# Kernel optimization log

Hardware: AMD Instinct MI355X
Metric: run time of the kernel (lower is better)

Reference implementation:

```python
import jax, jax.numpy as jnp
import numpy as np

B, T, D, S, ITERS = 32, 4096, 256, 8, 3
SCALE = D ** -0.5
EPS = 1e-8


def _ln(x, g, b):
    mu = jnp.mean(x, axis=-1, keepdims=True)
    var = jnp.var(x, axis=-1, keepdims=True)
    return (x - mu) / jnp.sqrt(var + 1e-5) * g + b


def setup_inputs() -> dict:
    key = jax.random.key(0)
    ks = jax.random.split(key, 16)
    w = lambda k, shp, s=0.02: jax.random.normal(k, shp, jnp.float32) * s
    return {
        "inputs": jax.random.normal(ks[0], (B, T, D), jnp.float32),
        "slots_mu": w(ks[1], (1, 1, D), 0.1),
        "slots_logsigma": w(ks[2], (1, 1, D), 0.1),
        "noise": jax.random.normal(ks[3], (B, S, D), jnp.float32),
        "Wq": w(ks[4], (D, D)),
        "Wk": w(ks[5], (D, D)),
        "Wv": w(ks[6], (D, D)),
        "norm_g": jnp.ones((D,), jnp.float32),
        "norm_b": jnp.zeros((D,), jnp.float32),
        "gru_wih": w(ks[7], (D, 3 * D)),
        "gru_whh": w(ks[8], (D, 3 * D)),
        "gru_bih": jnp.zeros((3 * D,), jnp.float32),
        "gru_bhh": jnp.zeros((3 * D,), jnp.float32),
        "mlp_ng": jnp.ones((D,), jnp.float32),
        "mlp_nb": jnp.zeros((D,), jnp.float32),
        "mlp_w1": w(ks[9], (D, 4 * D)),
        "mlp_b1": jnp.zeros((4 * D,), jnp.float32),
        "mlp_w2": w(ks[10], (4 * D, D)),
        "mlp_b2": jnp.zeros((D,), jnp.float32),
    }


def reference(inputs, slots_mu, slots_logsigma, noise, Wq, Wk, Wv, norm_g, norm_b,
              gru_wih, gru_whh, gru_bih, gru_bhh, mlp_ng, mlp_nb,
              mlp_w1, mlp_b1, mlp_w2, mlp_b2):
    # init slots: mu + sigma * noise, broadcast [1,1,D] -> [B,S,D]
    slots = slots_mu + jnp.exp(slots_logsigma) * noise

    keys = inputs @ Wk      # [B,T,D]
    values = inputs @ Wv    # [B,T,D]

    for _ in range(ITERS):
        slots_prev = slots
        s_n = _ln(slots, norm_g, norm_b)
        q = s_n @ Wq                                    # [B,S,D]
        dots = jnp.einsum('bsd,btd->bst', q, keys) * SCALE
        attn = jax.nn.softmax(dots, axis=1) + EPS       # softmax over slots
        attn = attn / jnp.sum(attn, axis=-1, keepdims=True)
        updates = jnp.einsum('bst,btd->bsd', attn, values)

        # GRUCell: x = updates, h = slots_prev (elementwise over B*S)
        gi = updates @ gru_wih + gru_bih                # [B,S,3D]
        gh = slots_prev @ gru_whh + gru_bhh
        ir, iz, inn = jnp.split(gi, 3, axis=-1)
        hr, hz, hn = jnp.split(gh, 3, axis=-1)
        r = jax.nn.sigmoid(ir + hr)
        z = jax.nn.sigmoid(iz + hz)
        n = jnp.tanh(inn + r * hn)
        slots = (1.0 - z) * n + z * slots_prev

        # pre-norm residual MLP
        h = _ln(slots, mlp_ng, mlp_nb)
        h = jax.nn.relu(h @ mlp_w1 + mlp_b1)
        slots = slots + (h @ mlp_w2 + mlp_b2)

    return slots
```

## Files before the change

### kernel.cpp

```cpp
#include <hip/hip_runtime.h>
#include <stdint.h>

#define B_ 32
#define T_ 4096
#define D_ 256
#define S_ 8
#define ITERS_ 3
#define SCALE_ 0.0625f
#define EPS_ 1e-8f
#define NCH 16
#define CHUNK (T_/NCH)

typedef short short8 __attribute__((ext_vector_type(8)));
typedef float f32x4 __attribute__((ext_vector_type(4)));

__device__ __forceinline__ uint32_t f2bf1(float x){
  union { float f; uint32_t u; } c; c.f = x;
  return (c.u + 0x7fffu + ((c.u >> 16) & 1u)) >> 16;
}
__device__ __forceinline__ uint32_t pack2bf(float a, float b){
  return f2bf1(a) | (f2bf1(b) << 16);
}
__device__ __forceinline__ float bflo(uint32_t u){ union{uint32_t u;float f;} c; c.u = u << 16; return c.f; }
__device__ __forceinline__ float bfhi(uint32_t u){ union{uint32_t u;float f;} c; c.u = u & 0xffff0000u; return c.f; }

__global__ void k_init(const float* __restrict__ mu, const float* __restrict__ ls,
                       const float* __restrict__ noise, float* __restrict__ slots){
  int i = blockIdx.x * 256 + threadIdx.x;
  int d = i & 255;
  slots[i] = mu[d] + __expf(ls[d]) * noise[i];
}

__global__ void k_wconv(const float* __restrict__ Wk, const float* __restrict__ Wv,
                        uint16_t* __restrict__ Wt){
  int n = blockIdx.x;
  int k = threadIdx.x;
  float v = (n < 256) ? Wk[k*256 + n] : Wv[k*256 + (n - 256)];
  Wt[n*256 + k] = (uint16_t)f2bf1(v);
}

__global__ void k_wq(const float* __restrict__ Wq, uint16_t* __restrict__ Wqt){
  int n = blockIdx.x, k = threadIdx.x;
  Wqt[n*256 + k] = (uint16_t)f2bf1(Wq[k*256 + n] * SCALE_);
}

__global__ void k_bcat(const float* __restrict__ wih, const float* __restrict__ whh,
                       uint16_t* __restrict__ Bcat){
  int n = blockIdx.x;
  int k = threadIdx.x;
  float v;
  if (n < 768) v = (k < 256) ? wih[k*768 + n] : whh[(k-256)*768 + n];
  else         v = (k < 256) ? 0.f            : whh[(k-256)*768 + 512 + (n-768)];
  Bcat[(size_t)n*512 + k] = (uint16_t)f2bf1(v);
}

__global__ void k_bc(const float* __restrict__ bih, const float* __restrict__ bhh,
                     float* __restrict__ bc){
  int i = blockIdx.x*256 + threadIdx.x;
  float v;
  if (i < 512) v = bih[i] + bhh[i];
  else if (i < 768) v = bih[i];
  else v = bhh[i - 256];
  bc[i] = v;
}

__global__ void k_w1t(const float* __restrict__ w1, uint16_t* __restrict__ w1t){
  int n = blockIdx.x, k = threadIdx.x;
  w1t[(size_t)n*256 + k] = (uint16_t)f2bf1(w1[(size_t)k*1024 + n]);
}
__global__ void k_w2t(const float* __restrict__ w2, uint16_t* __restrict__ w2t){
  int n = blockIdx.x, k0 = threadIdx.x;
  #pragma unroll
  for (int j = 0; j < 4; ++j){
    int k = j*256 + k0;
    w2t[(size_t)n*1024 + k] = (uint16_t)f2bf1(w2[(size_t)k*256 + n]);
  }
}

#define PPITCH 40
__global__ __launch_bounds__(256) void k_proj(const float* __restrict__ X,
                                              const uint16_t* __restrict__ Wt,
                                              uint16_t* __restrict__ Kp,
                                              uint16_t* __restrict__ Vp){
  __shared__ __align__(16) uint16_t As[128*PPITCH];
  __shared__ __align__(16) uint16_t Bs[128*PPITCH];
  __shared__ __align__(16) uint16_t Cs[128*128];
  int bid = blockIdx.x;
  int x = bid & 7, j = bid >> 3;
  int tau = 512*x + j;
  int mt = tau >> 2;
  int nt = tau & 3;
  int m0 = mt * 128;
  int n0 = nt * 128;
  int tid = threadIdx.x;
  int lane = tid & 63, wid = tid >> 6;
  int wm = wid >> 1, wn = wid & 1;
  int rsel = lane & 15, g = lane >> 4;

  f32x4 acc[4][4];
  for (int a = 0; a < 4; ++a)
    for (int b = 0; b < 4; ++b)
      acc[a][b] = (f32x4){0.f,0.f,0.f,0.f};

  for (int ks = 0; ks < 8; ++ks){
    int k0 = ks*32;
    #pragma unroll
    for (int i = 0; i < 2; ++i){
      int task = i*256 + tid;
      int row = task >> 2, seg = task & 3;
      const float* gp = X + (size_t)(m0 + row)*256 + k0 + seg*8;
      float4 a = *(const float4*)gp;
      float4 b = *(const float4*)(gp + 4);
      uint4 w;
      w.x = pack2bf(a.x, a.y); w.y = pack2bf(a.z, a.w);
      w.z = pack2bf(b.x, b.y); w.w = pack2bf(b.z, b.w);
      *(uint4*)&As[row*PPITCH + seg*8] = w;
    }
    #pragma unroll
    for (int i = 0; i < 2; ++i){
      int task = i*256 + tid;
      int row = task >> 2, seg = task & 3;
      uint4 v = *(const uint4*)(Wt + (size_t)(n0 + row)*256 + k0 + seg*8);
      *(uint4*)&Bs[row*PPITCH + seg*8] = v;
    }
    __syncthreads();
    short8 af[4], bfr[4];
    #pragma unroll
    for (int t = 0; t < 4; ++t)
      af[t] = *(const short8*)&As[(wm*64 + t*16 + rsel)*PPITCH + g*8];
    #pragma unroll
    for (int t = 0; t < 4; ++t)
      bfr[t] = *(const short8*)&Bs[(wn*64 + t*16 + rsel)*PPITCH + g*8];
    #pragma unroll
    for (int a = 0; a < 4; ++a)
      #pragma unroll
      for (int b = 0; b < 4; ++b)
        acc[a][b] = __builtin_amdgcn_mfma_f32_16x16x32_bf16(af[a], bfr[b], acc[a][b], 0, 0, 0);
    __syncthreads();
  }
  #pragma unroll
  for (int a = 0; a < 4; ++a)
    #pragma unroll
    for (int b = 0; b < 4; ++b)
      #pragma unroll
      for (int r = 0; r < 4; ++r){
        int mrow = wm*64 + a*16 + g*4 + r;
        int ncol = wn*64 + b*16 + rsel;
        Cs[mrow*128 + ncol] = (uint16_t)f2bf1(acc[a][b][r]);
      }
  __syncthreads();
  uint16_t* outp = (n0 < 256) ? Kp : Vp;
  int nbase = n0 & 255;
  #pragma unroll
  for (int i = 0; i < 4; ++i){
    int task = i*256 + tid;
    int row = task >> 3, seg = task & 7;
    uint4 v = *(uint4*)&Cs[row*128 + seg*16];
    *(uint4*)&outp[(size_t)(m0 + row)*256 + nbase + seg*16] = v;
  }
}

#define GPIT 40
template<int MODE>
__global__ __launch_bounds__(256) void k_gemm64(const uint16_t* __restrict__ A,
                                                const uint16_t* __restrict__ Bm,
                                                const float* __restrict__ bias,
                                                const float* __restrict__ resid,
                                                float* __restrict__ Cf,
                                                uint16_t* __restrict__ Cb,
                                                int N, int K){
  __shared__ __align__(16) uint16_t As[64*GPIT];
  __shared__ __align__(16) uint16_t Bs[64*GPIT];
  int m0 = blockIdx.y * 64, n0 = blockIdx.x * 64;
  int tid = threadIdx.x, lane = tid & 63, wid = tid >> 6;
  int wm = wid >> 1, wn = wid & 1;
  int rsel = lane & 15, g = lane >> 4;
  f32x4 acc[2][2];
  #pragma unroll
  for (int a = 0; a < 2; ++a)
    #pragma unroll
    for (int b = 0; b < 2; ++b)
      acc[a][b] = (f32x4){0.f,0.f,0.f,0.f};
  int row_s = tid >> 2, seg = tid & 3;
  for (int k0 = 0; k0 < K; k0 += 32){
    *(uint4*)&As[row_s*GPIT + seg*8] = *(const uint4*)(A  + (size_t)(m0+row_s)*K + k0 + seg*8);
    *(uint4*)&Bs[row_s*GPIT + seg*8] = *(const uint4*)(Bm + (size_t)(n0+row_s)*K + k0 + seg*8);
    __syncthreads();
    short8 af[2], bfr[2];
    #pragma unroll
    for (int t = 0; t < 2; ++t)
      af[t]  = *(const short8*)&As[(wm*32 + t*16 + rsel)*GPIT + g*8];
    #pragma unroll
    for (int t = 0; t < 2; ++t)
      bfr[t] = *(const short8*)&Bs[(wn*32 + t*16 + rsel)*GPIT + g*8];
    #pragma unroll
    for (int a = 0; a < 2; ++a)
      #pragma unroll
      for (int b = 0; b < 2; ++b)
        acc[a][b] = __builtin_amdgcn_mfma_f32_16x16x32_bf16(af[a], bfr[b], acc[a][b], 0, 0, 0);
    __syncthreads();
  }
  #pragma unroll
  for (int a = 0; a < 2; ++a)
    #pragma unroll
    for (int b = 0; b < 2; ++b)
      #pragma unroll
      for (int r = 0; r < 4; ++r){
        int mrow = m0 + wm*32 + a*16 + g*4 + r;
        int ncol = n0 + wn*32 + b*16 + rsel;
        float v = acc[a][b][r];
        if (MODE == 0) Cf[(size_t)mrow*N + ncol] = v;
        if (MODE == 1) Cb[(size_t)mrow*N + ncol] = (uint16_t)f2bf1(fmaxf(v + bias[ncol], 0.f));
        if (MODE == 2) Cf[(size_t)mrow*N + ncol] = v + bias[ncol] + resid[(size_t)mrow*N + ncol];
        if (MODE == 3) Cb[(size_t)mrow*N + ncol] = (uint16_t)f2bf1(v);
      }
}

__global__ __launch_bounds__(256) void k_ln(const float* __restrict__ src,
                                            const float* __restrict__ gg,
                                            const float* __restrict__ bb,
                                            uint16_t* __restrict__ dst){
  __shared__ float red[8];
  int row = blockIdx.x, tid = threadIdx.x;
  int lane = tid & 63, wid = tid >> 6;
  float xv = src[row*256 + tid];
  float s1 = xv, s2 = xv*xv;
  #pragma unroll
  for (int d = 32; d; d >>= 1){ s1 += __shfl_down(s1, d, 64); s2 += __shfl_down(s2, d, 64); }
  if (lane == 0){ red[wid] = s1; red[4 + wid] = s2; }
  __syncthreads();
  float mu = (red[0]+red[1]+red[2]+red[3]) * (1.f/256.f);
  float ms = (red[4]+red[5]+red[6]+red[7]) * (1.f/256.f);
  float rstd = rsqrtf(ms - mu*mu + 1e-5f);
  dst[row*256 + tid] = (uint16_t)f2bf1((xv - mu)*rstd*gg[tid] + bb[tid]);
}

__global__ __launch_bounds__(256) void k_gru_pre(const float* __restrict__ upd_part,
                                                 const float* __restrict__ sum_part,
                                                 const float* __restrict__ slots,
                                                 uint16_t* __restrict__ Acat){
  int row = blockIdx.x;
  int b = row >> 3, s = row & 7;
  int d = threadIdx.x;
  float sum = 0.f;
  #pragma unroll
  for (int ch = 0; ch < 16; ++ch) sum += sum_part[(size_t)(b*16 + ch)*8 + s];
  float acc = 0.f;
  #pragma unroll
  for (int ch = 0; ch < 16; ++ch) acc += upd_part[(size_t)(b*16 + ch)*2048 + s*256 + d];
  Acat[(size_t)row*512 + d]       = (uint16_t)f2bf1(acc / sum);
  Acat[(size_t)row*512 + 256 + d] = (uint16_t)f2bf1(slots[row*256 + d]);
}

__global__ __launch_bounds__(256) void k_combine(const float* __restrict__ G,
                                                 const float* __restrict__ bc,
                                                 const float* __restrict__ slots,
                                                 const float* __restrict__ mng,
                                                 const float* __restrict__ mnb,
                                                 float* __restrict__ s2f,
                                                 uint16_t* __restrict__ snb){
  __shared__ float red[8];
  int row = blockIdx.x, c = threadIdx.x;
  int lane = c & 63, wid = c >> 6;
  const float* Gr = G + (size_t)row*1024;
  float r  = 1.f / (1.f + __expf(-(Gr[c]       + bc[c])));
  float z  = 1.f / (1.f + __expf(-(Gr[256 + c] + bc[256 + c])));
  float Gn = Gr[512 + c], Gh = Gr[768 + c];
  float nn = tanhf((Gn - Gh + bc[512 + c]) + r*(Gh + bc[768 + c]));
  float hv = slots[row*256 + c];
  float s2 = (1.f - z)*nn + z*hv;
  s2f[row*256 + c] = s2;
  float p1 = s2, p2 = s2*s2;
  #pragma unroll
  for (int d = 32; d; d >>= 1){ p1 += __shfl_down(p1, d, 64); p2 += __shfl_down(p2, d, 64); }
  if (lane == 0){ red[wid] = p1; red[4 + wid] = p2; }
  __syncthreads();
  float mu = (red[0]+red[1]+red[2]+red[3]) * (1.f/256.f);
  float ms = (red[4]+red[5]+red[6]+red[7]) * (1.f/256.f);
  float rstd = rsqrtf(ms - mu*mu + 1e-5f);
  snb[row*256 + c] = (uint16_t)f2bf1((s2 - mu)*rstd*mng[c] + mnb[c]);
}

__global__ __launch_bounds__(256) void k_attn(const uint16_t* __restrict__ qbf,
                                              const uint16_t* __restrict__ Kp,
                                              const uint16_t* __restrict__ Vp,
                                              float* __restrict__ upd_part,
                                              float* __restrict__ sum_part){
  __shared__ __align__(16) uint16_t qs[16*264];
  __shared__ __align__(16) uint16_t Ks[64*264];
  __shared__ __align__(16) uint32_t attp[64*4];
  __shared__ float red[8*256];
  __shared__ float ssum[8];
  int bid = blockIdx.x;
  int b = bid >> 4, ch = bid & 15;
  int tid = threadIdx.x, lane = tid & 63, wid = tid >> 6;
  {
    const uint32_t* qg = (const uint32_t*)(qbf + (size_t)b*2048);
    uint32_t* qd = (uint32_t*)qs;
    #pragma unroll
    for (int i = 0; i < 4; ++i){
      int idx = i*256 + tid;
      int s = idx >> 7, c = idx & 127;
      qd[s*132 + c] = qg[idx];
    }
    #pragma unroll
    for (int i = 0; i < 5; ++i){
      int idx = i*256 + tid;
      if (idx < 1056) qd[8*132 + idx] = 0u;
    }
  }
  if (tid < 8) ssum[tid] = 0.f;
  __syncthreads();
  short8 aq[8];
  {
    int rs = lane & 15, g = lane >> 4;
    const char* qb = (const char*)qs;
    #pragma unroll
    for (int kk = 0; kk < 8; ++kk)
      aq[kk] = *(const short8*)(qb + rs*528 + kk*64 + g*16);
  }
  float upd[8][4];
  #pragma unroll
  for (int s = 0; s < 8; ++s){ upd[s][0]=0.f; upd[s][1]=0.f; upd[s][2]=0.f; upd[s][3]=0.f; }
  float sp[4] = {0.f,0.f,0.f,0.f};
  int dd = lane * 4;
  int tq = wid;

  for (int st = 0; st < 4; ++st){
    int t0 = ch*CHUNK + st*64;
    {
      const char* kg = (const char*)Kp + ((size_t)(b*T_ + t0) << 9);
      char* kd = (char*)Ks;
      #pragma unroll
      for (int i = 0; i < 8; ++i){
        int task = i*256 + tid;
        int row = task >> 5, seg = task & 31;
        uint4 v = *(const uint4*)(kg + (row << 9) + (seg << 4));
        *(uint4*)(kd + row*528 + seg*16) = v;
      }
    }
    __syncthreads();
    f32x4 dot = (f32x4){0.f,0.f,0.f,0.f};
    int col = lane & 15, g = lane >> 4;
    {
      const char* kb = (const char*)Ks + (wid*16 + col)*528 + g*16;
      #pragma unroll
      for (int kk = 0; kk < 8; ++kk){
        short8 bf = *(const short8*)(kb + kk*64);
        dot = __builtin_amdgcn_mfma_f32_16x16x32_bf16(aq[kk], bf, dot, 0, 0, 0);
      }
    }
    float x0 = dot[0], x1 = dot[1], x2 = dot[2], x3 = dot[3];
    float y0 = __shfl_xor(x0, 16, 64), y1 = __shfl_xor(x1, 16, 64);
    float y2 = __shfl_xor(x2, 16, 64), y3 = __shfl_xor(x3, 16, 64);
    float m = fmaxf(fmaxf(fmaxf(x0,x1), fmaxf(x2,x3)), fmaxf(fmaxf(y0,y1), fmaxf(y2,y3)));
    float e0 = __expf(x0-m), e1 = __expf(x1-m), e2 = __expf(x2-m), e3 = __expf(x3-m);
    float f0 = __expf(y0-m), f1 = __expf(y1-m), f2 = __expf(y2-m), f3 = __expf(y3-m);
    float inv = 1.f / (e0+e1+e2+e3+f0+f1+f2+f3);
    float p0 = e0*inv + EPS_, p1 = e1*inv + EPS_, p2 = e2*inv + EPS_, p3 = e3*inv + EPS_;
    if (g < 2){
      sp[0] += p0; sp[1] += p1; sp[2] += p2; sp[3] += p3;
      int t = wid*16 + col;
      attp[t*4 + g*2 + 0] = pack2bf(p0, p1);
      attp[t*4 + g*2 + 1] = pack2bf(p2, p3);
    }
    __syncthreads();
    {
      const char* vg = (const char*)Vp + ((size_t)(b*T_ + t0) << 9) + (size_t)dd*2;
      #pragma unroll
      for (int tt = 0; tt < 16; ++tt){
        int tl = tq*16 + tt;
        uint2 vv = *(const uint2*)(vg + ((size_t)tl << 9));
        uint4 aa = *(const uint4*)&attp[tl*4];
        float v0 = bflo(vv.x), v1 = bfhi(vv.x), v2 = bflo(vv.y), v3 = bfhi(vv.y);
        float av[8];
        av[0] = bflo(aa.x); av[1] = bfhi(aa.x); av[2] = bflo(aa.y); av[3] = bfhi(aa.y);
        av[4] = bflo(aa.z); av[5] = bfhi(aa.z); av[6] = bflo(aa.w); av[7] = bfhi(aa.w);
        #pragma unroll
        for (int s = 0; s < 8; ++s){
          upd[s][0] = fmaf(av[s], v0, upd[s][0]);
          upd[s][1] = fmaf(av[s], v1, upd[s][1]);
          upd[s][2] = fmaf(av[s], v2, upd[s][2]);
          upd[s][3] = fmaf(av[s], v3, upd[s][3]);
        }
      }
    }
    __syncthreads();
  }
  for (int ph = 0; ph < 4; ++ph){
    if (tq == ph){
      #pragma unroll
      for (int s = 0; s < 8; ++s)
        #pragma unroll
        for (int j2 = 0; j2 < 4; ++j2){
          if (ph == 0) red[s*256 + dd + j2]  = upd[s][j2];
          else         red[s*256 + dd + j2] += upd[s][j2];
        }
    }
    __syncthreads();
  }
  {
    float* up = upd_part + (size_t)bid * 2048;
    #pragma unroll
    for (int i = 0; i < 8; ++i) up[i*256 + tid] = red[i*256 + tid];
  }
  {
    int col = lane & 15, g = lane >> 4;
    #pragma unroll
    for (int dsh = 1; dsh < 16; dsh <<= 1){
      sp[0] += __shfl_xor(sp[0], dsh, 64); sp[1] += __shfl_xor(sp[1], dsh, 64);
      sp[2] += __shfl_xor(sp[2], dsh, 64); sp[3] += __shfl_xor(sp[3], dsh, 64);
    }
    if (col == 0 && g < 2){
      atomicAdd(&ssum[g*4 + 0], sp[0]);
      atomicAdd(&ssum[g*4 + 1], sp[1]);
      atomicAdd(&ssum[g*4 + 2], sp[2]);
      atomicAdd(&ssum[g*4 + 3], sp[3]);
    }
    __syncthreads();
    if (tid < 8) sum_part[(size_t)bid*8 + tid] = ssum[tid];
  }
}

extern "C" void kernel_launch(void* const* d_in, const int* in_sizes, int n_in,
                              void* d_out, int out_size, void* d_ws, size_t ws_size,
                              hipStream_t stream){
  const float* inputs = (const float*)d_in[0];
  const float* mu     = (const float*)d_in[1];
  const float* lsig   = (const float*)d_in[2];
  const float* noise  = (const float*)d_in[3];
  const float* Wq     = (const float*)d_in[4];
  const float* Wk     = (const float*)d_in[5];
  const float* Wv     = (const float*)d_in[6];
  const float* ng     = (const float*)d_in[7];
  const float* nb     = (const float*)d_in[8];
  const float* wih    = (const float*)d_in[9];
  const float* whh    = (const float*)d_in[10];
  const float* bih    = (const float*)d_in[11];
  const float* bhh    = (const float*)d_in[12];
  const float* mng    = (const float*)d_in[13];
  const float* mnb    = (const float*)d_in[14];
  const float* w1     = (const float*)d_in[15];
  const float* b1     = (const float*)d_in[16];
  const float* w2     = (const float*)d_in[17];
  const float* b2     = (const float*)d_in[18];
  float* slots = (float*)d_out;

  char* ws = (char*)d_ws;
  uint16_t* Wt       = (uint16_t*)(ws + 0);
  uint16_t* qbf      = (uint16_t*)(ws + 0x40000);
  float*    sum_part = (float*)   (ws + 0x60000);
  float*    upd_part = (float*)   (ws + 0x64000);
  uint16_t* Wqt      = (uint16_t*)(ws + 0x480000);
  uint16_t* Bcat     = (uint16_t*)(ws + 0x4A0000);
  uint16_t* w1t      = (uint16_t*)(ws + 0x5A0000);
  uint16_t* w2t      = (uint16_t*)(ws + 0x620000);
  float*    bc       = (float*)   (ws + 0x6A0000);
  uint16_t* Acat     = (uint16_t*)(ws + 0x6B0000);
  float*    G        = (float*)   (ws + 0x6F0000);
  uint16_t* snb      = (uint16_t*)(ws + 0x7F0000);
  float*    s2f      = (float*)   (ws + 0x810000);
  uint16_t* h1b      = (uint16_t*)(ws + 0x850000);
  uint16_t* lnb      = (uint16_t*)(ws + 0x8D0000);
  uint16_t* Kp       = (uint16_t*)(ws + 0x1000000);
  uint16_t* Vp       = (uint16_t*)(ws + 0x5000000);

  hipLaunchKernelGGL(k_init,  dim3(256),  dim3(256), 0, stream, mu, lsig, noise, slots);
  hipLaunchKernelGGL(k_wconv, dim3(512),  dim3(256), 0, stream, Wk, Wv, Wt);
  hipLaunchKernelGGL(k_wq,    dim3(256),  dim3(256), 0, stream, Wq, Wqt);
  hipLaunchKernelGGL(k_bcat,  dim3(1024), dim3(512), 0, stream, wih, whh, Bcat);
  hipLaunchKernelGGL(k_bc,    dim3(4),    dim3(256), 0, stream, bih, bhh, bc);
  hipLaunchKernelGGL(k_w1t,   dim3(1024), dim3(256), 0, stream, w1, w1t);
  hipLaunchKernelGGL(k_w2t,   dim3(256),  dim3(256), 0, stream, w2, w2t);
  hipLaunchKernelGGL(k_proj,  dim3(4096), dim3(256), 0, stream, inputs, Wt, Kp, Vp);

  for (int it = 0; it < ITERS_; ++it){
    hipLaunchKernelGGL(k_ln,        dim3(256), dim3(256), 0, stream, slots, ng, nb, lnb);
    hipLaunchKernelGGL(k_gemm64<3>, dim3(4,4),  dim3(256), 0, stream, lnb, Wqt,
                       (const float*)nullptr, (const float*)nullptr, (float*)nullptr, qbf, 256, 256);
    hipLaunchKernelGGL(k_attn,      dim3(512), dim3(256), 0, stream, qbf, Kp, Vp, upd_part, sum_part);
    hipLaunchKernelGGL(k_gru_pre,   dim3(256), dim3(256), 0, stream, upd_part, sum_part, slots, Acat);
    hipLaunchKernelGGL(k_gemm64<0>, dim3(16,4), dim3(256), 0, stream, Acat, Bcat,
                       (const float*)nullptr, (const float*)nullptr, G, (uint16_t*)nullptr, 1024, 512);
    hipLaunchKernelGGL(k_combine,   dim3(256), dim3(256), 0, stream, G, bc, slots, mng, mnb, s2f, snb);
    hipLaunchKernelGGL(k_gemm64<1>, dim3(16,4), dim3(256), 0, stream, snb, w1t,
                       b1, (const float*)nullptr, (float*)nullptr, h1b, 1024, 256);
    hipLaunchKernelGGL(k_gemm64<2>, dim3(4,4),  dim3(256), 0, stream, h1b, w2t,
                       b2, s2f, slots, (uint16_t*)nullptr, 256, 1024);
  }
}
```

Measured before the change: 526.5 us.

## Fuse prep kernels, LN+Q projection, and two-layer MLP; use hardware bf16 convert

Merges the seven weight-preparation and slot-init kernels into one launch. Fuses the layernorm with the Q projection, and the two MLP GEMMs (with ReLU and residual) into single kernels that keep the hidden activations in shared memory. The input conversion in the K/V projection now uses the v_cvt_pk_bf16_f32 instruction instead of software rounding. This cuts kernel launches and global round trips for the small per-iteration stages, but the fused kernels run on only 16 blocks, which limits parallelism.

```diff
diff --git a/kernel.cpp b/kernel.cpp
--- a/kernel.cpp
+++ b/kernel.cpp
@@ -21,59 +21,67 @@
 __device__ __forceinline__ uint32_t pack2bf(float a, float b){
   return f2bf1(a) | (f2bf1(b) << 16);
 }
+__device__ __forceinline__ uint32_t cvtpk2bf(float a, float b){
+  uint32_t r;
+  asm("v_cvt_pk_bf16_f32 %0, %1, %2" : "=v"(r) : "v"(a), "v"(b));
+  return r;
+}
 __device__ __forceinline__ float bflo(uint32_t u){ union{uint32_t u;float f;} c; c.u = u << 16; return c.f; }
 __device__ __forceinline__ float bfhi(uint32_t u){ union{uint32_t u;float f;} c; c.u = u & 0xffff0000u; return c.f; }
 
-__global__ void k_init(const float* __restrict__ mu, const float* __restrict__ ls,
-                       const float* __restrict__ noise, float* __restrict__ slots){
-  int i = blockIdx.x * 256 + threadIdx.x;
-  int d = i & 255;
-  slots[i] = mu[d] + __expf(ls[d]) * noise[i];
-}
-
-__global__ void k_wconv(const float* __restrict__ Wk, const float* __restrict__ Wv,
-                        uint16_t* __restrict__ Wt){
-  int n = blockIdx.x;
-  int k = threadIdx.x;
-  float v = (n < 256) ? Wk[k*256 + n] : Wv[k*256 + (n - 256)];
-  Wt[n*256 + k] = (uint16_t)f2bf1(v);
-}
-
-__global__ void k_wq(const float* __restrict__ Wq, uint16_t* __restrict__ Wqt){
-  int n = blockIdx.x, k = threadIdx.x;
-  Wqt[n*256 + k] = (uint16_t)f2bf1(Wq[k*256 + n] * SCALE_);
-}
-
-__global__ void k_bcat(const float* __restrict__ wih, const float* __restrict__ whh,
-                       uint16_t* __restrict__ Bcat){
-  int n = blockIdx.x;
-  int k = threadIdx.x;
-  float v;
-  if (n < 768) v = (k < 256) ? wih[k*768 + n] : whh[(k-256)*768 + n];
-  else         v = (k < 256) ? 0.f            : whh[(k-256)*768 + 512 + (n-768)];
-  Bcat[(size_t)n*512 + k] = (uint16_t)f2bf1(v);
-}
-
-__global__ void k_bc(const float* __restrict__ bih, const float* __restrict__ bhh,
-                     float* __restrict__ bc){
-  int i = blockIdx.x*256 + threadIdx.x;
-  float v;
-  if (i < 512) v = bih[i] + bhh[i];
-  else if (i < 768) v = bih[i];
-  else v = bhh[i - 256];
-  bc[i] = v;
-}
-
-__global__ void k_w1t(const float* __restrict__ w1, uint16_t* __restrict__ w1t){
-  int n = blockIdx.x, k = threadIdx.x;
-  w1t[(size_t)n*256 + k] = (uint16_t)f2bf1(w1[(size_t)k*1024 + n]);
-}
-__global__ void k_w2t(const float* __restrict__ w2, uint16_t* __restrict__ w2t){
-  int n = blockIdx.x, k0 = threadIdx.x;
-  #pragma unroll
-  for (int j = 0; j < 4; ++j){
-    int k = j*256 + k0;
-    w2t[(size_t)n*1024 + k] = (uint16_t)f2bf1(w2[(size_t)k*256 + n]);
+__global__ __launch_bounds__(256) void k_prep(const float* __restrict__ Wk, const float* __restrict__ Wv,
+                                              const float* __restrict__ Wq,
+                                              const float* __restrict__ wih, const float* __restrict__ whh,
+                                              const float* __restrict__ bih, const float* __restrict__ bhh,
+                                              const float* __restrict__ w1, const float* __restrict__ w2,
+                                              const float* __restrict__ mu, const float* __restrict__ ls,
+                                              const float* __restrict__ noise,
+                                              uint16_t* __restrict__ Wt, uint16_t* __restrict__ Wqt,
+                                              uint16_t* __restrict__ Bcat, float* __restrict__ bc,
+                                              uint16_t* __restrict__ w1t, uint16_t* __restrict__ w2t,
+                                              float* __restrict__ slots){
+  int g = blockIdx.x, tid = threadIdx.x;
+  if (g < 512){
+    int n = g, k = tid;
+    float v = (n < 256) ? Wk[k*256 + n] : Wv[k*256 + (n - 256)];
+    Wt[n*256 + k] = (uint16_t)f2bf1(v);
+  } else if (g < 768){
+    int n = g - 512, k = tid;
+    Wqt[n*256 + k] = (uint16_t)f2bf1(Wq[k*256 + n] * SCALE_);
+  } else if (g < 1792){
+    int n = g - 768;
+    #pragma unroll
+    for (int j = 0; j < 2; ++j){
+      int k = j*256 + tid;
+      float v;
+      if (n < 768) v = (k < 256) ? wih[k*768 + n] : whh[(k-256)*768 + n];
+      else         v = (k < 256) ? 0.f            : whh[(k-256)*768 + 512 + (n-768)];
+      Bcat[(size_t)n*512 + k] = (uint16_t)f2bf1(v);
+    }
+  } else if (g < 1793){
+    #pragma unroll
+    for (int j = 0; j < 4; ++j){
+      int i = j*256 + tid;
+      float v;
+      if (i < 512) v = bih[i] + bhh[i];
+      else if (i < 768) v = bih[i];
+      else v = bhh[i - 256];
+      bc[i] = v;
+    }
+  } else if (g < 2817){
+    int n = g - 1793, k = tid;
+    w1t[(size_t)n*256 + k] = (uint16_t)f2bf1(w1[(size_t)k*1024 + n]);
+  } else if (g < 3073){
+    int n = g - 2817;
+    #pragma unroll
+    for (int j = 0; j < 4; ++j){
+      int k = j*256 + tid;
+      w2t[(size_t)n*1024 + k] = (uint16_t)f2bf1(w2[(size_t)k*256 + n]);
+    }
+  } else {
+    int i = (g - 3073)*256 + tid;
+    int d = i & 255;
+    slots[i] = mu[d] + __expf(ls[d]) * noise[i];
   }
 }
 
@@ -112,8 +120,8 @@
       float4 a = *(const float4*)gp;
       float4 b = *(const float4*)(gp + 4);
       uint4 w;
-      w.x = pack2bf(a.x, a.y); w.y = pack2bf(a.z, a.w);
-      w.z = pack2bf(b.x, b.y); w.w = pack2bf(b.z, b.w);
+      w.x = cvtpk2bf(a.x, a.y); w.y = cvtpk2bf(a.z, a.w);
+      w.z = cvtpk2bf(b.x, b.y); w.w = cvtpk2bf(b.z, b.w);
       *(uint4*)&As[row*PPITCH + seg*8] = w;
     }
     #pragma unroll
@@ -160,17 +168,75 @@
   }
 }
 
+__global__ __launch_bounds__(256) void k_qln(const float* __restrict__ slots,
+                                             const uint16_t* __restrict__ Wqt,
+                                             const float* __restrict__ ng,
+                                             const float* __restrict__ nb,
+                                             uint16_t* __restrict__ qbf){
+  __shared__ __align__(16) uint16_t snl[16*264];
+  int m0 = blockIdx.x * 16;
+  int tid = threadIdx.x;
+  int r = tid >> 4, cs = (tid & 15) * 16;
+  float xv[16];
+  {
+    const float* sp = slots + (size_t)(m0 + r)*256 + cs;
+    #pragma unroll
+    for (int i = 0; i < 4; ++i){
+      float4 v = *(const float4*)(sp + i*4);
+      xv[i*4+0]=v.x; xv[i*4+1]=v.y; xv[i*4+2]=v.z; xv[i*4+3]=v.w;
+    }
+  }
+  float s1 = 0.f, s2 = 0.f;
+  #pragma unroll
+  for (int i = 0; i < 16; ++i){ s1 += xv[i]; s2 += xv[i]*xv[i]; }
+  #pragma unroll
+  for (int m = 1; m < 16; m <<= 1){ s1 += __shfl_xor(s1, m, 64); s2 += __shfl_xor(s2, m, 64); }
+  float mu = s1 * (1.f/256.f);
+  float ms = s2 * (1.f/256.f);
+  float rstd = rsqrtf(ms - mu*mu + 1e-5f);
+  {
+    uint32_t pk[8];
+    #pragma unroll
+    for (int i = 0; i < 8; ++i){
+      float a = (xv[2*i]   - mu)*rstd*ng[cs+2*i]   + nb[cs+2*i];
+      float b = (xv[2*i+1] - mu)*rstd*ng[cs+2*i+1] + nb[cs+2*i+1];
+      pk[i] = pack2bf(a, b);
+    }
+    uint4* dst = (uint4*)&snl[r*264 + cs];
+    dst[0] = (uint4){pk[0],pk[1],pk[2],pk[3]};
+    dst[1] = (uint4){pk[4],pk[5],pk[6],pk[7]};
+  }
+  __syncthreads();
+  int lane = tid & 63, w = tid >> 6;
+  int rsel = lane & 15, g = lane >> 4;
+  short8 aq[8];
+  #pragma unroll
+  for (int kk = 0; kk < 8; ++kk)
+    aq[kk] = *(const short8*)((const char*)snl + rsel*528 + kk*64 + g*16);
+  int n0w = w*64;
+  #pragma unroll
+  for (int nt = 0; nt < 4; ++nt){
+    f32x4 acc = (f32x4){0.f,0.f,0.f,0.f};
+    #pragma unroll
+    for (int kk = 0; kk < 8; ++kk){
+      short8 bfr = *(const short8*)&Wqt[(size_t)(n0w + nt*16 + rsel)*256 + kk*32 + g*8];
+      acc = __builtin_amdgcn_mfma_f32_16x16x32_bf16(aq[kk], bfr, acc, 0, 0, 0);
+    }
+    #pragma unroll
+    for (int r4 = 0; r4 < 4; ++r4){
+      int row = g*4 + r4;
+      qbf[(size_t)(m0 + row)*256 + n0w + nt*16 + rsel] = (uint16_t)f2bf1(acc[r4]);
+    }
+  }
+}
+
 #define GPIT 40
-template<int MODE>
-__global__ __launch_bounds__(256) void k_gemm64(const uint16_t* __restrict__ A,
-                                                const uint16_t* __restrict__ Bm,
-                                                const float* __restrict__ bias,
-                                                const float* __restrict__ resid,
-                                                float* __restrict__ Cf,
-                                                uint16_t* __restrict__ Cb,
-                                                int N, int K){
+__global__ __launch_bounds__(256) void k_gemmG(const uint16_t* __restrict__ A,
+                                               const uint16_t* __restrict__ Bm,
+                                               float* __restrict__ Cf){
   __shared__ __align__(16) uint16_t As[64*GPIT];
   __shared__ __align__(16) uint16_t Bs[64*GPIT];
+  const int N = 1024, K = 512;
   int m0 = blockIdx.y * 64, n0 = blockIdx.x * 64;
   int tid = threadIdx.x, lane = tid & 63, wid = tid >> 6;
   int wm = wid >> 1, wn = wid & 1;
@@ -208,31 +274,8 @@
       for (int r = 0; r < 4; ++r){
         int mrow = m0 + wm*32 + a*16 + g*4 + r;
         int ncol = n0 + wn*32 + b*16 + rsel;
-        float v = acc[a][b][r];
-        if (MODE == 0) Cf[(size_t)mrow*N + ncol] = v;
-        if (MODE == 1) Cb[(size_t)mrow*N + ncol] = (uint16_t)f2bf1(fmaxf(v + bias[ncol], 0.f));
-        if (MODE == 2) Cf[(size_t)mrow*N + ncol] = v + bias[ncol] + resid[(size_t)mrow*N + ncol];
-        if (MODE == 3) Cb[(size_t)mrow*N + ncol] = (uint16_t)f2bf1(v);
+        Cf[(size_t)mrow*N + ncol] = acc[a][b][r];
       }
-}
-
-__global__ __launch_bounds__(256) void k_ln(const float* __restrict__ src,
-                                            const float* __restrict__ gg,
-                                            const float* __restrict__ bb,
-                                            uint16_t* __restrict__ dst){
-  __shared__ float red[8];
-  int row = blockIdx.x, tid = threadIdx.x;
-  int lane = tid & 63, wid = tid >> 6;
-  float xv = src[row*256 + tid];
-  float s1 = xv, s2 = xv*xv;
-  #pragma unroll
-  for (int d = 32; d; d >>= 1){ s1 += __shfl_down(s1, d, 64); s2 += __shfl_down(s2, d, 64); }
-  if (lane == 0){ red[wid] = s1; red[4 + wid] = s2; }
-  __syncthreads();
-  float mu = (red[0]+red[1]+red[2]+red[3]) * (1.f/256.f);
-  float ms = (red[4]+red[5]+red[6]+red[7]) * (1.f/256.f);
-  float rstd = rsqrtf(ms - mu*mu + 1e-5f);
-  dst[row*256 + tid] = (uint16_t)f2bf1((xv - mu)*rstd*gg[tid] + bb[tid]);
 }
 
 __global__ __launch_bounds__(256) void k_gru_pre(const float* __restrict__ upd_part,
@@ -279,6 +322,62 @@
   float ms = (red[4]+red[5]+red[6]+red[7]) * (1.f/256.f);
   float rstd = rsqrtf(ms - mu*mu + 1e-5f);
   snb[row*256 + c] = (uint16_t)f2bf1((s2 - mu)*rstd*mng[c] + mnb[c]);
+}
+
+#define HPIT 1048
+__global__ __launch_bounds__(256) void k_mlp(const uint16_t* __restrict__ snb,
+                                             const uint16_t* __restrict__ w1t,
+                                             const float* __restrict__ b1,
+                                             const uint16_t* __restrict__ w2t,
+                                             const float* __restrict__ b2,
+                                             const float* __restrict__ s2f,
+                                             float* __restrict__ slots){
+  __shared__ __align__(16) uint16_t h1s[16*HPIT];
+  int m0 = blockIdx.x * 16;
+  int tid = threadIdx.x, lane = tid & 63, w = tid >> 6;
+  int rsel = lane & 15, g = lane >> 4;
+  short8 aq[8];
+  #pragma unroll
+  for (int kk = 0; kk < 8; ++kk)
+    aq[kk] = *(const short8*)&snb[(size_t)(m0 + rsel)*256 + kk*32 + g*8];
+  #pragma unroll
+  for (int nt = 0; nt < 16; ++nt){
+    int ncol = w*256 + nt*16 + rsel;
+    f32x4 acc = (f32x4){0.f,0.f,0.f,0.f};
+    #pragma unroll
+    for (int kk = 0; kk < 8; ++kk){
+      short8 bfr = *(const short8*)&w1t[(size_t)ncol*256 + kk*32 + g*8];
+      acc = __builtin_amdgcn_mfma_f32_16x16x32_bf16(aq[kk], bfr, acc, 0, 0, 0);
+    }
+    float bv = b1[ncol];
+    #pragma unroll
+    for (int r4 = 0; r4 < 4; ++r4){
+      int row = g*4 + r4;
+      h1s[row*HPIT + ncol] = (uint16_t)f2bf1(fmaxf(acc[r4] + bv, 0.f));
+    }
+  }
+  __syncthreads();
+  f32x4 acc2[4];
+  #pragma unroll
+  for (int nt = 0; nt < 4; ++nt) acc2[nt] = (f32x4){0.f,0.f,0.f,0.f};
+  for (int kk = 0; kk < 32; ++kk){
+    short8 aq2 = *(const short8*)((const char*)h1s + rsel*2096 + kk*64 + g*16);
+    #pragma unroll
+    for (int nt = 0; nt < 4; ++nt){
+      short8 bfr = *(const short8*)&w2t[(size_t)(w*64 + nt*16 + rsel)*1024 + kk*32 + g*8];
+      acc2[nt] = __builtin_amdgcn_mfma_f32_16x16x32_bf16(aq2, bfr, acc2[nt], 0, 0, 0);
+    }
+  }
+  #pragma unroll
+  for (int nt = 0; nt < 4; ++nt){
+    int ncol = w*64 + nt*16 + rsel;
+    float bv = b2[ncol];
+    #pragma unroll
+    for (int r4 = 0; r4 < 4; ++r4){
+      int row = m0 + g*4 + r4;
+      slots[(size_t)row*256 + ncol] = s2f[(size_t)row*256 + ncol] + acc2[nt][r4] + bv;
+    }
+  }
 }
 
 __global__ __launch_bounds__(256) void k_attn(const uint16_t* __restrict__ qbf,
@@ -460,32 +559,20 @@
   float*    G        = (float*)   (ws + 0x6F0000);
   uint16_t* snb      = (uint16_t*)(ws + 0x7F0000);
   float*    s2f      = (float*)   (ws + 0x810000);
-  uint16_t* h1b      = (uint16_t*)(ws + 0x850000);
-  uint16_t* lnb      = (uint16_t*)(ws + 0x8D0000);
   uint16_t* Kp       = (uint16_t*)(ws + 0x1000000);
   uint16_t* Vp       = (uint16_t*)(ws + 0x5000000);
 
-  hipLaunchKernelGGL(k_init,  dim3(256),  dim3(256), 0, stream, mu, lsig, noise, slots);
-  hipLaunchKernelGGL(k_wconv, dim3(512),  dim3(256), 0, stream, Wk, Wv, Wt);
-  hipLaunchKernelGGL(k_wq,    dim3(256),  dim3(256), 0, stream, Wq, Wqt);
-  hipLaunchKernelGGL(k_bcat,  dim3(1024), dim3(512), 0, stream, wih, whh, Bcat);
-  hipLaunchKernelGGL(k_bc,    dim3(4),    dim3(256), 0, stream, bih, bhh, bc);
-  hipLaunchKernelGGL(k_w1t,   dim3(1024), dim3(256), 0, stream, w1, w1t);
-  hipLaunchKernelGGL(k_w2t,   dim3(256),  dim3(256), 0, stream, w2, w2t);
-  hipLaunchKernelGGL(k_proj,  dim3(4096), dim3(256), 0, stream, inputs, Wt, Kp, Vp);
+  hipLaunchKernelGGL(k_prep, dim3(3329), dim3(256), 0, stream,
+                     Wk, Wv, Wq, wih, whh, bih, bhh, w1, w2, mu, lsig, noise,
+                     Wt, Wqt, Bcat, bc, w1t, w2t, slots);
+  hipLaunchKernelGGL(k_proj, dim3(4096), dim3(256), 0, stream, inputs, Wt, Kp, Vp);
 
   for (int it = 0; it < ITERS_; ++it){
-    hipLaunchKernelGGL(k_ln,        dim3(256), dim3(256), 0, stream, slots, ng, nb, lnb);
-    hipLaunchKernelGGL(k_gemm64<3>, dim3(4,4),  dim3(256), 0, stream, lnb, Wqt,
-                       (const float*)nullptr, (const float*)nullptr, (float*)nullptr, qbf, 256, 256);
-    hipLaunchKernelGGL(k_attn,      dim3(512), dim3(256), 0, stream, qbf, Kp, Vp, upd_part, sum_part);
-    hipLaunchKernelGGL(k_gru_pre,   dim3(256), dim3(256), 0, stream, upd_part, sum_part, slots, Acat);
-    hipLaunchKernelGGL(k_gemm64<0>, dim3(16,4), dim3(256), 0, stream, Acat, Bcat,
-                       (const float*)nullptr, (const float*)nullptr, G, (uint16_t*)nullptr, 1024, 512);
-    hipLaunchKernelGGL(k_combine,   dim3(256), dim3(256), 0, stream, G, bc, slots, mng, mnb, s2f, snb);
-    hipLaunchKernelGGL(k_gemm64<1>, dim3(16,4), dim3(256), 0, stream, snb, w1t,
-                       b1, (const float*)nullptr, (float*)nullptr, h1b, 1024, 256);
-    hipLaunchKernelGGL(k_gemm64<2>, dim3(4,4),  dim3(256), 0, stream, h1b, w2t,
-                       b2, s2f, slots, (uint16_t*)nullptr, 256, 1024);
-  }
-}
+    hipLaunchKernelGGL(k_qln,     dim3(16),   dim3(256), 0, stream, slots, Wqt, ng, nb, qbf);
+    hipLaunchKernelGGL(k_attn,    dim3(512),  dim3(256), 0, stream, qbf, Kp, Vp, upd_part, sum_part);
+    hipLaunchKernelGGL(k_gru_pre, dim3(256),  dim3(256), 0, stream, upd_part, sum_part, slots, Acat);
+    hipLaunchKernelGGL(k_gemmG,   dim3(16,4), dim3(256), 0, stream, Acat, Bcat, G);
+    hipLaunchKernelGGL(k_combine, dim3(256),  dim3(256), 0, stream, G, bc, slots, mng, mnb, s2f, snb);
+    hipLaunchKernelGGL(k_mlp,     dim3(16),   dim3(256), 0, stream, snb, w1t, b1, w2t, b2, s2f, slots);
+  }
+}
```

New measurement: 645.2 us. 1.23x slower.
